# Kernel optimization log

Measured on AMD Instinct MI355X. Metric: run time of the kernel, lower is better.

The kernel has to match this reference:

```python
import jax, jax.numpy as jnp
import numpy as np

D = 128      # d_model
H = 8        # n_heads
HD = D // H  # head_dim = 16
E = 256      # n_experts
R = 32       # kv_lora_rank
B, T = 4, 512
EPS = 1e-6


def _dense_init(k, fi, fo):
    s = float(1.0 / np.sqrt(fi))
    return jax.random.uniform(k, (fi, fo), minval=-s, maxval=s, dtype=jnp.float32)


def setup_inputs() -> dict:
    key = jax.random.key(0)
    ks = jax.random.split(key, 16)
    rng = np.random.RandomState(42)
    Q, _ = np.linalg.qr(rng.randn(D, D))
    glim = float(np.sqrt(6.0 / (D + D)))
    return {
        'x': jax.random.normal(ks[0], (B, T, D), dtype=jnp.float32),
        'g1': jnp.ones((D,), jnp.float32),
        'qW': _dense_init(ks[1], D, D), 'qb': jnp.zeros((D,), jnp.float32),
        'kdW': _dense_init(ks[2], D, R), 'kdb': jnp.zeros((R,), jnp.float32),
        'kuW': _dense_init(ks[3], R, 2 * D), 'kub': jnp.zeros((2 * D,), jnp.float32),
        'oW': _dense_init(ks[4], D, D), 'ob': jnp.zeros((D,), jnp.float32),
        'rot': jnp.asarray(Q, jnp.float32),
        'tq_scale': jnp.ones((D,), jnp.float32),
        's1W': _dense_init(ks[5], D, D), 's1b': jnp.zeros((D,), jnp.float32),
        's2W': _dense_init(ks[6], D, D), 's2b': jnp.zeros((D,), jnp.float32),
        'g2': jnp.ones((D,), jnp.float32),
        'gateW': _dense_init(ks[7], D, E), 'gateb': jnp.zeros((E,), jnp.float32),
        'expW': jax.random.uniform(ks[8], (E, D, D), minval=-glim, maxval=glim, dtype=jnp.float32),
        'm1W': _dense_init(ks[9], D, D), 'm1b': jnp.zeros((D,), jnp.float32),
        'm2W': _dense_init(ks[10], D, D), 'm2b': jnp.zeros((D,), jnp.float32),
    }


def _rmsnorm(x, g):
    return g * (x / jnp.sqrt(jnp.mean(x * x, axis=-1, keepdims=True) + EPS))


def _swiglu(x, w1, b1, w2, b2):
    gate = x @ w1 + b1
    return gate * jax.nn.sigmoid(gate) * (x @ w2 + b2)


def _mla(x, qW, qb, kdW, kdb, kuW, kub, oW, ob):
    b, t = x.shape[0], x.shape[1]
    q = (x @ qW + qb).reshape(b, t, H, HD)
    kv = ((x @ kdW + kdb) @ kuW + kub).reshape(b, t, H, 2 * HD)
    k, v = jnp.split(kv, 2, axis=-1)
    q = jax.nn.elu(q) + 1.0
    k = jax.nn.elu(k) + 1.0
    # linear attention: context[b,h,d,e] = sum_t k[b,t,h,d] v[b,t,h,e]
    context = jnp.einsum('bthd,bthe->bhde', k, v)
    out = jnp.einsum('bthd,bhde->bthe', q, context)
    k_sum = jnp.sum(k, axis=1)  # [b,h,d]
    z = 1.0 / (jnp.einsum('bthd,bhd->bth', q, k_sum) + EPS)
    out = out * z[..., None]
    return out.reshape(b, t, D) @ oW + ob


def _turbo_quant(x, rot, scale):
    x = x @ rot
    mag = jnp.sqrt(jnp.mean(x * x, axis=-1, keepdims=True) + EPS)
    phase = x / mag
    qp = jnp.clip(phase * 127.0, -127.0, 127.0) / 127.0
    phase = jax.lax.stop_gradient(qp - phase) + phase  # straight-through
    return phase * mag * scale


def _moe(h, gateW, gateb, expW, m1W, m1b, m2W, m2b):
    gate_scores = jax.nn.softmax(h @ gateW + gateb, axis=-1)  # [B,T,E]
    top_vals, top_idx = jax.lax.top_k(gate_scores, 2)
    top_w = top_vals / (jnp.sum(top_vals, axis=-1, keepdims=True) + EPS)
    # dense all-expert compute as in the original module
    eo = jnp.einsum('btd,edo->bteo', h, expW)  # [B,T,E,D]
    mask = jnp.sum(jax.nn.one_hot(top_idx, E, dtype=h.dtype) * top_w[..., None], axis=2)  # [B,T,E]
    wavg = jnp.einsum('bteo,bte->bto', eo, mask)
    wavg = _swiglu(wavg, m1W, m1b, m2W, m2b)
    diff_sq = jnp.square(eo - wavg[:, :, None, :])
    wvar = jnp.einsum('bteo,bte->bto', diff_sq, mask)
    consensus = jnp.exp(-jnp.mean(wvar, axis=-1))  # [B,T]
    return wavg, consensus


def reference(x, g1, qW, qb, kdW, kdb, kuW, kub, oW, ob, rot, tq_scale,
              s1W, s1b, s2W, s2b, g2, gateW, gateb, expW, m1W, m1b, m2W, m2b):
    attn_out = _turbo_quant(_mla(_rmsnorm(x, g1), qW, qb, kdW, kdb, kuW, kub, oW, ob), rot, tq_scale)
    x = x + _swiglu(attn_out, s1W, s1b, s2W, s2b)
    moe_out, consensus = _moe(_rmsnorm(x, g2), gateW, gateb, expW, m1W, m1b, m2W, m2b)
    return x + moe_out, consensus
```

## Files before the change

### kernel.cpp

```cpp
#include <hip/hip_runtime.h>
#include <hip/hip_bf16.h>
#include <math.h>

static constexpr int Dd   = 128;
static constexpr int NH   = 8;
static constexpr int HD   = 16;
static constexpr int NE   = 256;
static constexpr int RR   = 32;
static constexpr int BB   = 4;
static constexpr int TT   = 512;
static constexpr int NTOK = BB * TT;
static constexpr int TPB  = 4;
#define EPSF 1e-6f

__device__ __forceinline__ float elu1(float v) { return v > 0.f ? v + 1.f : expf(v); }
__device__ __forceinline__ float sigm(float v) { return 1.f / (1.f + expf(-v)); }

__global__ __launch_bounds__(256) void k_pre(
    const float* __restrict__ x, const float* __restrict__ g1,
    const float* __restrict__ qW, const float* __restrict__ qb,
    const float* __restrict__ kdW, const float* __restrict__ kdb,
    const float* __restrict__ kuW, const float* __restrict__ kub,
    float* __restrict__ qbuf, float* __restrict__ kvbuf,
    float* __restrict__ ctx, float* __restrict__ ksum, int* __restrict__ cnt) {
  const int tid = threadIdx.x;
  const int j = tid & 127, g = tid >> 7;
  const int lane = tid & 63, wid = tid >> 6;
  const int n0 = blockIdx.x * TPB;

  __shared__ float4 h1T[128];
  __shared__ float4 part0[128];
  __shared__ float4 kpart[4][32];
  __shared__ float4 kdT[32];
  __shared__ float4 rtmp[2];

  if (blockIdx.x == 0) {
    for (int i = tid; i < 32 * 256; i += 256) ctx[i] = 0.f;
    for (int i = tid; i < 32 * 16; i += 256) ksum[i] = 0.f;
    cnt[tid] = 0;
  }

  float xv[4];
  if (g == 0) {
    float v[4];
#pragma unroll
    for (int t = 0; t < 4; t++) { xv[t] = x[(n0 + t) * Dd + j]; v[t] = xv[t] * xv[t]; }
#pragma unroll
    for (int o = 32; o > 0; o >>= 1) {
#pragma unroll
      for (int t = 0; t < 4; t++) v[t] += __shfl_xor(v[t], o, 64);
    }
    if (lane == 0) rtmp[wid] = make_float4(v[0], v[1], v[2], v[3]);
  }
  __syncthreads();
  if (g == 0) {
    float g1j = g1[j];
#pragma unroll
    for (int t = 0; t < 4; t++) {
      float ss = ((const float*)&rtmp[0])[t] + ((const float*)&rtmp[1])[t];
      ((float*)&h1T[j])[t] = g1j * xv[t] * rsqrtf(ss * (1.f / 128.f) + EPSF);
    }
  }
  __syncthreads();

  {
    float a0 = 0, a1 = 0, a2 = 0, a3 = 0;
    const float* Wp = qW + (g * 64) * Dd + j;
#pragma unroll 8
    for (int i = 0; i < 64; i++) {
      float4 h4 = h1T[g * 64 + i];
      float w = Wp[i * Dd];
      a0 += h4.x * w; a1 += h4.y * w; a2 += h4.z * w; a3 += h4.w * w;
    }
    if (g == 1) part0[j] = make_float4(a0, a1, a2, a3);
    __syncthreads();
    if (g == 0) {
      float4 p = part0[j];
      float bb = qb[j];
      float q0 = a0 + p.x + bb, q1 = a1 + p.y + bb, q2 = a2 + p.z + bb, q3 = a3 + p.w + bb;
      qbuf[(n0 + 0) * Dd + j] = elu1(q0);
      qbuf[(n0 + 1) * Dd + j] = elu1(q1);
      qbuf[(n0 + 2) * Dd + j] = elu1(q2);
      qbuf[(n0 + 3) * Dd + j] = elu1(q3);
    }
  }

  if (tid < 128) {
    int col = tid & 31, ksp = tid >> 5;
    float a0 = 0, a1 = 0, a2 = 0, a3 = 0;
    const float* Wp = kdW + (ksp * 32) * RR + col;
#pragma unroll 8
    for (int i = 0; i < 32; i++) {
      float4 h4 = h1T[ksp * 32 + i];
      float w = Wp[i * RR];
      a0 += h4.x * w; a1 += h4.y * w; a2 += h4.z * w; a3 += h4.w * w;
    }
    kpart[ksp][col] = make_float4(a0, a1, a2, a3);
  }
  __syncthreads();
  if (tid < 32) {
    float bb = kdb[tid];
    float4 p0 = kpart[0][tid], p1 = kpart[1][tid], p2 = kpart[2][tid], p3 = kpart[3][tid];
    kdT[tid] = make_float4(p0.x + p1.x + p2.x + p3.x + bb,
                           p0.y + p1.y + p2.y + p3.y + bb,
                           p0.z + p1.z + p2.z + p3.z + bb,
                           p0.w + p1.w + p2.w + p3.w + bb);
  }
  __syncthreads();

  {
    float a0 = 0, a1 = 0, a2 = 0, a3 = 0;
    const float* Wp = kuW + tid;
#pragma unroll 8
    for (int r = 0; r < 32; r++) {
      float4 k4 = kdT[r];
      float w = Wp[r * 256];
      a0 += k4.x * w; a1 += k4.y * w; a2 += k4.z * w; a3 += k4.w * w;
    }
    float bb = kub[tid];
    bool isk = (tid & 31) < 16;
    float v0 = a0 + bb, v1 = a1 + bb, v2 = a2 + bb, v3 = a3 + bb;
    kvbuf[(n0 + 0) * 256 + tid] = isk ? elu1(v0) : v0;
    kvbuf[(n0 + 1) * 256 + tid] = isk ? elu1(v1) : v1;
    kvbuf[(n0 + 2) * 256 + tid] = isk ? elu1(v2) : v2;
    kvbuf[(n0 + 3) * 256 + tid] = isk ? elu1(v3) : v3;
  }
}

__global__ __launch_bounds__(256) void k_ctx(const float* __restrict__ kv,
                                             float* __restrict__ ctx,
                                             float* __restrict__ ksum) {
  const int blk = blockIdx.x;
  const int bh = blk >> 3, c = blk & 7;
  const int b = bh >> 3, h = bh & 7;
  const int tid = threadIdx.x;
  const int d = tid >> 4, e = tid & 15;
  __shared__ float sh[64 * 32];
#pragma unroll
  for (int r = 0; r < 8; r++) {
    int lin = r * 256 + tid;
    int tok = lin >> 5, off = lin & 31;
    sh[lin] = kv[((b * TT + c * 64 + tok) * 256) + h * 32 + off];
  }
  __syncthreads();
  float acc = 0.f, ks = 0.f;
#pragma unroll 4
  for (int t = 0; t < 64; t++) {
    float kk = sh[t * 32 + d];
    acc += kk * sh[t * 32 + 16 + e];
    ks += kk;
  }
  atomicAdd(&ctx[bh * 256 + d * 16 + e], acc);
  if (e == 0) atomicAdd(&ksum[bh * 16 + d], ks);
}

__global__ __launch_bounds__(256) void k_mid(
    const float* __restrict__ x, const float* __restrict__ qbuf,
    const float* __restrict__ ctx, const float* __restrict__ ksum,
    const float* __restrict__ oW, const float* __restrict__ ob,
    const float* __restrict__ rot, const float* __restrict__ tqs,
    const float* __restrict__ s1W, const float* __restrict__ s1b,
    const float* __restrict__ s2W, const float* __restrict__ s2b,
    const float* __restrict__ g2, const float* __restrict__ gateW,
    const float* __restrict__ gateb,
    float* __restrict__ xnbuf, float* __restrict__ h2buf,
    float* __restrict__ gw, int* __restrict__ gidx, int* __restrict__ cnt) {
  const int tid = threadIdx.x;
  const int j = tid & 127, g = tid >> 7;
  const int lane = tid & 63, wid2 = (tid >> 6) & 1;
  const int wid4 = tid >> 6;
  const int n0 = blockIdx.x * TPB;
  const int b = n0 >> 9;

  __shared__ float4 bufA[128], bufB[128];
  __shared__ float4 part[2][128];
  __shared__ float4 rtmp[2];
  __shared__ float wvS[4][4]; __shared__ int wiS[4][4];
  __shared__ float zS[4][4];

  {
    float a = qbuf[(n0 + 2 * g) * Dd + j];
    float c = qbuf[(n0 + 2 * g + 1) * Dd + j];
    ((float*)&bufA[j])[2 * g] = a;
    ((float*)&bufA[j])[2 * g + 1] = c;
  }
  __syncthreads();

  if (g == 0) {
    int h = j >> 4, e = j & 15;
    const float* cpt = ctx + (b * NH + h) * 256;
    const float* kpt = ksum + (b * NH + h) * 16;
    float num[4] = {0, 0, 0, 0}, den[4] = {0, 0, 0, 0};
#pragma unroll
    for (int d = 0; d < 16; d++) {
      float cx = cpt[d * 16 + e], ks = kpt[d];
      float4 q4 = bufA[h * 16 + d];
      num[0] += q4.x * cx; num[1] += q4.y * cx; num[2] += q4.z * cx; num[3] += q4.w * cx;
      den[0] += q4.x * ks; den[1] += q4.y * ks; den[2] += q4.z * ks; den[3] += q4.w * ks;
    }
#pragma unroll
    for (int t = 0; t < 4; t++) ((float*)&bufB[j])[t] = num[t] / (den[t] + EPSF);
  }
  __syncthreads();

  {
    float a0 = 0, a1 = 0, a2 = 0, a3 = 0;
    const float* Wp = oW + (g * 64) * Dd + j;
#pragma unroll 8
    for (int i = 0; i < 64; i++) {
      float4 h4 = bufB[g * 64 + i];
      float w = Wp[i * Dd];
      a0 += h4.x * w; a1 += h4.y * w; a2 += h4.z * w; a3 += h4.w * w;
    }
    if (g == 1) part[0][j] = make_float4(a0, a1, a2, a3);
    __syncthreads();
    if (g == 0) {
      float4 p = part[0][j];
      float bb = ob[j];
      bufA[j] = make_float4(a0 + p.x + bb, a1 + p.y + bb, a2 + p.z + bb, a3 + p.w + bb);
    }
    __syncthreads();
  }

  {
    float a0 = 0, a1 = 0, a2 = 0, a3 = 0;
    const float* Wp = rot + (g * 64) * Dd + j;
#pragma unroll 8
    for (int i = 0; i < 64; i++) {
      float4 h4 = bufA[g * 64 + i];
      float w = Wp[i * Dd];
      a0 += h4.x * w; a1 += h4.y * w; a2 += h4.z * w; a3 += h4.w * w;
    }
    if (g == 1) part[0][j] = make_float4(a0, a1, a2, a3);
    __syncthreads();
    float tot[4];
    if (g == 0) {
      float4 p = part[0][j];
      tot[0] = a0 + p.x; tot[1] = a1 + p.y; tot[2] = a2 + p.z; tot[3] = a3 + p.w;
      float v[4];
#pragma unroll
      for (int t = 0; t < 4; t++) v[t] = tot[t] * tot[t];
#pragma unroll
      for (int o = 32; o > 0; o >>= 1) {
#pragma unroll
        for (int t = 0; t < 4; t++) v[t] += __shfl_xor(v[t], o, 64);
      }
      if (lane == 0) rtmp[wid2] = make_float4(v[0], v[1], v[2], v[3]);
    }
    __syncthreads();
    if (g == 0) {
      float scj = tqs[j];
#pragma unroll
      for (int t = 0; t < 4; t++) {
        float ss = ((const float*)&rtmp[0])[t] + ((const float*)&rtmp[1])[t];
        float mag = sqrtf(ss * (1.f / 128.f) + EPSF);
        float ph = tot[t] / mag;
        float p127 = fminf(fmaxf(ph * 127.f, -127.f), 127.f);
        ((float*)&bufB[j])[t] = (p127 * (1.f / 127.f)) * mag * scj;
      }
    }
    __syncthreads();
  }

  {
    float a1v[4] = {0, 0, 0, 0}, a2v[4] = {0, 0, 0, 0};
    const float* W1p = s1W + (g * 64) * Dd + j;
    const float* W2p = s2W + (g * 64) * Dd + j;
#pragma unroll 4
    for (int i = 0; i < 64; i++) {
      float4 h4 = bufB[g * 64 + i];
      float w1 = W1p[i * Dd], w2 = W2p[i * Dd];
      a1v[0] += h4.x * w1; a1v[1] += h4.y * w1; a1v[2] += h4.z * w1; a1v[3] += h4.w * w1;
      a2v[0] += h4.x * w2; a2v[1] += h4.y * w2; a2v[2] += h4.z * w2; a2v[3] += h4.w * w2;
    }
    if (g == 1) {
      part[0][j] = make_float4(a1v[0], a1v[1], a1v[2], a1v[3]);
      part[1][j] = make_float4(a2v[0], a2v[1], a2v[2], a2v[3]);
    }
    __syncthreads();
    float xn[4];
    if (g == 0) {
      float b1 = s1b[j], b2 = s2b[j];
      float4 p1 = part[0][j], p2 = part[1][j];
      float gv[4], uv[4];
      gv[0] = a1v[0] + p1.x + b1; gv[1] = a1v[1] + p1.y + b1;
      gv[2] = a1v[2] + p1.z + b1; gv[3] = a1v[3] + p1.w + b1;
      uv[0] = a2v[0] + p2.x + b2; uv[1] = a2v[1] + p2.y + b2;
      uv[2] = a2v[2] + p2.z + b2; uv[3] = a2v[3] + p2.w + b2;
      float v[4];
#pragma unroll
      for (int t = 0; t < 4; t++) {
        xn[t] = x[(n0 + t) * Dd + j] + gv[t] * sigm(gv[t]) * uv[t];
        xnbuf[(n0 + t) * Dd + j] = xn[t];
        v[t] = xn[t] * xn[t];
      }
#pragma unroll
      for (int o = 32; o > 0; o >>= 1) {
#pragma unroll
        for (int t = 0; t < 4; t++) v[t] += __shfl_xor(v[t], o, 64);
      }
      if (lane == 0) rtmp[wid2] = make_float4(v[0], v[1], v[2], v[3]);
    }
    __syncthreads();
    if (g == 0) {
      float g2j = g2[j];
#pragma unroll
      for (int t = 0; t < 4; t++) {
        float ss = ((const float*)&rtmp[0])[t] + ((const float*)&rtmp[1])[t];
        float h2v = g2j * xn[t] * rsqrtf(ss * (1.f / 128.f) + EPSF);
        ((float*)&bufA[j])[t] = h2v;
        h2buf[(n0 + t) * Dd + j] = h2v;
      }
    }
    __syncthreads();
  }

  float val[4];
  {
    float a0 = 0, a1 = 0, a2 = 0, a3 = 0;
    const float* Wp = gateW + tid;
#pragma unroll 8
    for (int i = 0; i < 128; i++) {
      float4 h4 = bufA[i];
      float w = Wp[i * NE];
      a0 += h4.x * w; a1 += h4.y * w; a2 += h4.z * w; a3 += h4.w * w;
    }
    float bb = gateb[tid];
    val[0] = a0 + bb; val[1] = a1 + bb; val[2] = a2 + bb; val[3] = a3 + bb;
  }

  float m1[4]; int i1[4];
  {
    float bv[4]; int bi[4];
#pragma unroll
    for (int t = 0; t < 4; t++) { bv[t] = val[t]; bi[t] = tid; }
#pragma unroll
    for (int o = 32; o > 0; o >>= 1) {
#pragma unroll
      for (int t = 0; t < 4; t++) {
        float wv = __shfl_xor(bv[t], o, 64);
        int wi = __shfl_xor(bi[t], o, 64);
        if (wv > bv[t] || (wv == bv[t] && wi < bi[t])) { bv[t] = wv; bi[t] = wi; }
      }
    }
    if (lane == 0) {
#pragma unroll
      for (int t = 0; t < 4; t++) { wvS[wid4][t] = bv[t]; wiS[wid4][t] = bi[t]; }
    }
    __syncthreads();
#pragma unroll
    for (int t = 0; t < 4; t++) {
      m1[t] = wvS[0][t]; i1[t] = wiS[0][t];
#pragma unroll
      for (int w = 1; w < 4; w++) {
        float cv = wvS[w][t]; int ci = wiS[w][t];
        if (cv > m1[t] || (cv == m1[t] && ci < i1[t])) { m1[t] = cv; i1[t] = ci; }
      }
    }
    __syncthreads();
  }
  float m2[4]; int i2[4];
  {
    float bv[4]; int bi[4];
#pragma unroll
    for (int t = 0; t < 4; t++) {
      bv[t] = (tid == i1[t]) ? -INFINITY : val[t];
      bi[t] = tid;
    }
#pragma unroll
    for (int o = 32; o > 0; o >>= 1) {
#pragma unroll
      for (int t = 0; t < 4; t++) {
        float wv = __shfl_xor(bv[t], o, 64);
        int wi = __shfl_xor(bi[t], o, 64);
        if (wv > bv[t] || (wv == bv[t] && wi < bi[t])) { bv[t] = wv; bi[t] = wi; }
      }
    }
    if (lane == 0) {
#pragma unroll
      for (int t = 0; t < 4; t++) { wvS[wid4][t] = bv[t]; wiS[wid4][t] = bi[t]; }
    }
    __syncthreads();
#pragma unroll
    for (int t = 0; t < 4; t++) {
      m2[t] = wvS[0][t]; i2[t] = wiS[0][t];
#pragma unroll
      for (int w = 1; w < 4; w++) {
        float cv = wvS[w][t]; int ci = wiS[w][t];
        if (cv > m2[t] || (cv == m2[t] && ci < i2[t])) { m2[t] = cv; i2[t] = ci; }
      }
    }
    __syncthreads();
  }
  {
    float v[4];
#pragma unroll
    for (int t = 0; t < 4; t++) v[t] = expf(val[t] - m1[t]);
#pragma unroll
    for (int o = 32; o > 0; o >>= 1) {
#pragma unroll
      for (int t = 0; t < 4; t++) v[t] += __shfl_xor(v[t], o, 64);
    }
    if (lane == 0) {
#pragma unroll
      for (int t = 0; t < 4; t++) zS[wid4][t] = v[t];
    }
    __syncthreads();
  }
  if (tid < 4) {
    int t = tid;
    float Z = zS[0][t] + zS[1][t] + zS[2][t] + zS[3][t];
    float p1 = 1.f / Z;
    float p2 = expf(m2[t] - m1[t]) / Z;
    float s = p1 + p2 + EPSF;
    gidx[(n0 + t) * 2 + 0] = i1[t];
    gidx[(n0 + t) * 2 + 1] = i2[t];
    gw[(n0 + t) * 2 + 0] = p1 / s;
    gw[(n0 + t) * 2 + 1] = p2 / s;
    atomicAdd(&cnt[i1[t]], 1);
    atomicAdd(&cnt[i2[t]], 1);
  }
}

__global__ __launch_bounds__(256) void k_route(const int* __restrict__ cnt,
                                               const int* __restrict__ gidx,
                                               int* __restrict__ offb,
                                               int* __restrict__ slottok,
                                               int* __restrict__ tokslot) {
  const int tid = threadIdx.x;
  __shared__ int sc[256];
  __shared__ int lcur[256];
  int c = cnt[tid];
  sc[tid] = c;
  __syncthreads();
  for (int o = 1; o < 256; o <<= 1) {
    int a = (tid >= o) ? sc[tid - o] : 0;
    __syncthreads();
    sc[tid] += a;
    __syncthreads();
  }
  int excl = sc[tid] - c;
  offb[tid] = excl;
  lcur[tid] = excl;
  __syncthreads();
  for (int base = 0; base < NTOK; base += 256) {
    int tok = base + tid;
    int e1 = gidx[tok * 2], e2 = gidx[tok * 2 + 1];
    int s1 = atomicAdd(&lcur[e1], 1);
    tokslot[tok * 2] = s1; slottok[s1] = tok;
    int s2 = atomicAdd(&lcur[e2], 1);
    tokslot[tok * 2 + 1] = s2; slottok[s2] = tok;
  }
}

__global__ __launch_bounds__(256) void k_exp(const float* __restrict__ h2buf,
                                             const int* __restrict__ slottok,
                                             const int* __restrict__ cnt,
                                             const int* __restrict__ offb,
                                             const float* __restrict__ expW,
                                             float* __restrict__ ybuf) {
  const int e = blockIdx.x;
  const int n = cnt[e];
  if (n == 0) return;
  const int base = offb[e];
  const int tid = threadIdx.x;
  const int j = tid & 127, g = tid >> 7;
  __shared__ __align__(16) float hT[128][16];
  const float* Wp = expW + (size_t)e * Dd * Dd + j;
  for (int t0 = 0; t0 < n; t0 += 16) {
    int m = n - t0; if (m > 16) m = 16;
    __syncthreads();
    for (int tt = g; tt < m; tt += 2) {
      int tok = slottok[base + t0 + tt];
      hT[j][tt] = h2buf[tok * Dd + j];
    }
    __syncthreads();
    float acc[8] = {0, 0, 0, 0, 0, 0, 0, 0};
#pragma unroll 4
    for (int i = 0; i < 128; i++) {
      float w = Wp[i * Dd];
      const float* hp = &hT[i][g * 8];
      float4 A = *(const float4*)(hp);
      float4 B = *(const float4*)(hp + 4);
      acc[0] += A.x * w; acc[1] += A.y * w; acc[2] += A.z * w; acc[3] += A.w * w;
      acc[4] += B.x * w; acc[5] += B.y * w; acc[6] += B.z * w; acc[7] += B.w * w;
    }
#pragma unroll
    for (int k = 0; k < 8; k++) {
      int tt = g * 8 + k;
      if (tt < m) ybuf[(size_t)(base + t0 + tt) * Dd + j] = acc[k];
    }
  }
}

__global__ __launch_bounds__(256) void k_post(
    const float* __restrict__ xnbuf, const float* __restrict__ ybuf,
    const int* __restrict__ tokslot, const float* __restrict__ gw,
    const float* __restrict__ m1W, const float* __restrict__ m1b,
    const float* __restrict__ m2W, const float* __restrict__ m2b,
    float* __restrict__ out) {
  const int tid = threadIdx.x;
  const int j = tid & 127, g = tid >> 7;
  const int lane = tid & 63, wid2 = (tid >> 6) & 1;
  const int n0 = blockIdx.x * TPB;

  __shared__ float4 y1T[128], y2T[128], inT[128], sT[128];
  __shared__ float4 part[2][128];
  __shared__ float4 rtmp[2];
  __shared__ int sSlot[4][2];
  __shared__ float sWt[4][2];

  if (tid < 4) {
    sSlot[tid][0] = tokslot[(n0 + tid) * 2];
    sSlot[tid][1] = tokslot[(n0 + tid) * 2 + 1];
    sWt[tid][0] = gw[(n0 + tid) * 2];
    sWt[tid][1] = gw[(n0 + tid) * 2 + 1];
  }
  __syncthreads();

#pragma unroll
  for (int tt = 0; tt < 2; tt++) {
    int t = 2 * g + tt;
    float y1 = ybuf[(size_t)sSlot[t][0] * Dd + j];
    float y2 = ybuf[(size_t)sSlot[t][1] * Dd + j];
    ((float*)&y1T[j])[t] = y1;
    ((float*)&y2T[j])[t] = y2;
    ((float*)&inT[j])[t] = sWt[t][0] * y1 + sWt[t][1] * y2;
  }
  __syncthreads();

  {
    float a1v[4] = {0, 0, 0, 0}, a2v[4] = {0, 0, 0, 0};
    const float* W1p = m1W + (g * 64) * Dd + j;
    const float* W2p = m2W + (g * 64) * Dd + j;
#pragma unroll 4
    for (int i = 0; i < 64; i++) {
      float4 h4 = inT[g * 64 + i];
      float w1 = W1p[i * Dd], w2 = W2p[i * Dd];
      a1v[0] += h4.x * w1; a1v[1] += h4.y * w1; a1v[2] += h4.z * w1; a1v[3] += h4.w * w1;
      a2v[0] += h4.x * w2; a2v[1] += h4.y * w2; a2v[2] += h4.z * w2; a2v[3] += h4.w * w2;
    }
    if (g == 1) {
      part[0][j] = make_float4(a1v[0], a1v[1], a1v[2], a1v[3]);
      part[1][j] = make_float4(a2v[0], a2v[1], a2v[2], a2v[3]);
    }
    __syncthreads();
    if (g == 0) {
      float b1 = m1b[j], b2 = m2b[j];
      float4 p1 = part[0][j], p2 = part[1][j];
      float gv[4], uv[4];
      gv[0] = a1v[0] + p1.x + b1; gv[1] = a1v[1] + p1.y + b1;
      gv[2] = a1v[2] + p1.z + b1; gv[3] = a1v[3] + p1.w + b1;
      uv[0] = a2v[0] + p2.x + b2; uv[1] = a2v[1] + p2.y + b2;
      uv[2] = a2v[2] + p2.z + b2; uv[3] = a2v[3] + p2.w + b2;
#pragma unroll
      for (int t = 0; t < 4; t++) {
        float sv = gv[t] * sigm(gv[t]) * uv[t];
        ((float*)&sT[j])[t] = sv;
        out[(n0 + t) * Dd + j] = xnbuf[(n0 + t) * Dd + j] + sv;
      }
    }
    __syncthreads();
  }

  if (g == 0) {
    float v[4];
#pragma unroll
    for (int t = 0; t < 4; t++) {
      float sv = ((const float*)&sT[j])[t];
      float d1 = ((const float*)&y1T[j])[t] - sv;
      float d2 = ((const float*)&y2T[j])[t] - sv;
      v[t] = sWt[t][0] * d1 * d1 + sWt[t][1] * d2 * d2;
    }
#pragma unroll
    for (int o = 32; o > 0; o >>= 1) {
#pragma unroll
      for (int t = 0; t < 4; t++) v[t] += __shfl_xor(v[t], o, 64);
    }
    if (lane == 0) rtmp[wid2] = make_float4(v[0], v[1], v[2], v[3]);
  }
  __syncthreads();
  if (tid < 4) {
    float s = ((const float*)&rtmp[0])[tid] + ((const float*)&rtmp[1])[tid];
    out[NTOK * Dd + n0 + tid] = expf(-s * (1.f / 128.f));
  }
}

extern "C" void kernel_launch(void* const* d_in, const int* in_sizes, int n_in,
                              void* d_out, int out_size, void* d_ws, size_t ws_size,
                              hipStream_t stream) {
  const float* x   = (const float*)d_in[0];
  const float* g1  = (const float*)d_in[1];
  const float* qW  = (const float*)d_in[2];
  const float* qb  = (const float*)d_in[3];
  const float* kdW = (const float*)d_in[4];
  const float* kdb = (const float*)d_in[5];
  const float* kuW = (const float*)d_in[6];
  const float* kub = (const float*)d_in[7];
  const float* oW  = (const float*)d_in[8];
  const float* ob  = (const float*)d_in[9];
  const float* rot = (const float*)d_in[10];
  const float* tqs = (const float*)d_in[11];
  const float* s1W = (const float*)d_in[12];
  const float* s1b = (const float*)d_in[13];
  const float* s2W = (const float*)d_in[14];
  const float* s2b = (const float*)d_in[15];
  const float* g2  = (const float*)d_in[16];
  const float* gW  = (const float*)d_in[17];
  const float* gb  = (const float*)d_in[18];
  const float* eW  = (const float*)d_in[19];
  const float* m1W = (const float*)d_in[20];
  const float* m1b = (const float*)d_in[21];
  const float* m2W = (const float*)d_in[22];
  const float* m2b = (const float*)d_in[23];
  float* out = (float*)d_out;
  float* ws  = (float*)d_ws;

  float* qbuf  = ws;
  float* kvbuf = ws + 262144;
  float* ybuf  = ws;
  float* ctx   = ws + 786432;
  float* ksum  = ctx + 8192;
  float* h2buf = ksum + 512;
  float* xnbuf = h2buf + 262144;
  float* gw    = xnbuf + 262144;
  int*   gidx    = (int*)(gw + 4096);
  int*   cnt     = gidx + 4096;
  int*   offb    = cnt + 256;
  int*   slottok = offb + 256;
  int*   tokslot = slottok + 4096;

  k_pre<<<NTOK / TPB, 256, 0, stream>>>(x, g1, qW, qb, kdW, kdb, kuW, kub,
                                        qbuf, kvbuf, ctx, ksum, cnt);
  k_ctx<<<256, 256, 0, stream>>>(kvbuf, ctx, ksum);
  k_mid<<<NTOK / TPB, 256, 0, stream>>>(x, qbuf, ctx, ksum, oW, ob, rot, tqs,
                                        s1W, s1b, s2W, s2b, g2, gW, gb,
                                        xnbuf, h2buf, gw, gidx, cnt);
  k_route<<<1, 256, 0, stream>>>(cnt, gidx, offb, slottok, tokslot);
  k_exp<<<NE, 256, 0, stream>>>(h2buf, slottok, cnt, offb, eW, ybuf);
  k_post<<<NTOK / TPB, 256, 0, stream>>>(xnbuf, ybuf, tokslot, gw,
                                         m1W, m1b, m2W, m2b, out);
}
```

Before: 195.5 us.

## Double block size to 512 threads with wider K-split reductions

Four kernels (pre, mid, exp, post) move from 256 to 512 threads per block. Each matvec's K dimension is split across four thread groups instead of two, with partial sums reduced through shared memory. The expert GEMM gives each thread 4 tokens instead of 8 and pads its shared tile stride to 20. The aim is more parallel work per block to hide the latency of the serial matvec chains, at the cost of extra shared-memory reductions, more barriers and idle threads in the top-k and softmax stages.

```diff
diff --git a/kernel.cpp b/kernel.cpp
--- a/kernel.cpp
+++ b/kernel.cpp
@@ -16,7 +16,7 @@
 __device__ __forceinline__ float elu1(float v) { return v > 0.f ? v + 1.f : expf(v); }
 __device__ __forceinline__ float sigm(float v) { return 1.f / (1.f + expf(-v)); }
 
-__global__ __launch_bounds__(256) void k_pre(
+__global__ __launch_bounds__(512) void k_pre(
     const float* __restrict__ x, const float* __restrict__ g1,
     const float* __restrict__ qW, const float* __restrict__ qb,
     const float* __restrict__ kdW, const float* __restrict__ kdb,
@@ -25,23 +25,24 @@
     float* __restrict__ ctx, float* __restrict__ ksum, int* __restrict__ cnt) {
   const int tid = threadIdx.x;
   const int j = tid & 127, g = tid >> 7;
-  const int lane = tid & 63, wid = tid >> 6;
+  const int lane = tid & 63;
   const int n0 = blockIdx.x * TPB;
 
   __shared__ float4 h1T[128];
-  __shared__ float4 part0[128];
-  __shared__ float4 kpart[4][32];
+  __shared__ float4 part[3][128];
+  __shared__ float4 kpart[8][32];
   __shared__ float4 kdT[32];
+  __shared__ float4 kupart[256];
   __shared__ float4 rtmp[2];
 
   if (blockIdx.x == 0) {
-    for (int i = tid; i < 32 * 256; i += 256) ctx[i] = 0.f;
-    for (int i = tid; i < 32 * 16; i += 256) ksum[i] = 0.f;
-    cnt[tid] = 0;
+    for (int i = tid; i < 32 * 256; i += 512) ctx[i] = 0.f;
+    ksum[tid] = 0.f;
+    if (tid < 256) cnt[tid] = 0;
   }
 
   float xv[4];
-  if (g == 0) {
+  if (tid < 128) {
     float v[4];
 #pragma unroll
     for (int t = 0; t < 4; t++) { xv[t] = x[(n0 + t) * Dd + j]; v[t] = xv[t] * xv[t]; }
@@ -50,10 +51,10 @@
 #pragma unroll
       for (int t = 0; t < 4; t++) v[t] += __shfl_xor(v[t], o, 64);
     }
-    if (lane == 0) rtmp[wid] = make_float4(v[0], v[1], v[2], v[3]);
-  }
-  __syncthreads();
-  if (g == 0) {
+    if (lane == 0) rtmp[tid >> 6] = make_float4(v[0], v[1], v[2], v[3]);
+  }
+  __syncthreads();
+  if (tid < 128) {
     float g1j = g1[j];
 #pragma unroll
     for (int t = 0; t < 4; t++) {
@@ -65,33 +66,33 @@
 
   {
     float a0 = 0, a1 = 0, a2 = 0, a3 = 0;
-    const float* Wp = qW + (g * 64) * Dd + j;
-#pragma unroll 8
-    for (int i = 0; i < 64; i++) {
-      float4 h4 = h1T[g * 64 + i];
+    const float* Wp = qW + (g * 32) * Dd + j;
+#pragma unroll 16
+    for (int i = 0; i < 32; i++) {
+      float4 h4 = h1T[g * 32 + i];
       float w = Wp[i * Dd];
       a0 += h4.x * w; a1 += h4.y * w; a2 += h4.z * w; a3 += h4.w * w;
     }
-    if (g == 1) part0[j] = make_float4(a0, a1, a2, a3);
+    if (g) part[g - 1][j] = make_float4(a0, a1, a2, a3);
     __syncthreads();
     if (g == 0) {
-      float4 p = part0[j];
+      float4 p0 = part[0][j], p1 = part[1][j], p2 = part[2][j];
       float bb = qb[j];
-      float q0 = a0 + p.x + bb, q1 = a1 + p.y + bb, q2 = a2 + p.z + bb, q3 = a3 + p.w + bb;
-      qbuf[(n0 + 0) * Dd + j] = elu1(q0);
-      qbuf[(n0 + 1) * Dd + j] = elu1(q1);
-      qbuf[(n0 + 2) * Dd + j] = elu1(q2);
-      qbuf[(n0 + 3) * Dd + j] = elu1(q3);
-    }
-  }
-
-  if (tid < 128) {
+      qbuf[(n0 + 0) * Dd + j] = elu1(a0 + p0.x + p1.x + p2.x + bb);
+      qbuf[(n0 + 1) * Dd + j] = elu1(a1 + p0.y + p1.y + p2.y + bb);
+      qbuf[(n0 + 2) * Dd + j] = elu1(a2 + p0.z + p1.z + p2.z + bb);
+      qbuf[(n0 + 3) * Dd + j] = elu1(a3 + p0.w + p1.w + p2.w + bb);
+    }
+    __syncthreads();
+  }
+
+  if (tid < 256) {
     int col = tid & 31, ksp = tid >> 5;
     float a0 = 0, a1 = 0, a2 = 0, a3 = 0;
-    const float* Wp = kdW + (ksp * 32) * RR + col;
-#pragma unroll 8
-    for (int i = 0; i < 32; i++) {
-      float4 h4 = h1T[ksp * 32 + i];
+    const float* Wp = kdW + (ksp * 16) * RR + col;
+#pragma unroll
+    for (int i = 0; i < 16; i++) {
+      float4 h4 = h1T[ksp * 16 + i];
       float w = Wp[i * RR];
       a0 += h4.x * w; a1 += h4.y * w; a2 += h4.z * w; a3 += h4.w * w;
     }
@@ -100,30 +101,38 @@
   __syncthreads();
   if (tid < 32) {
     float bb = kdb[tid];
-    float4 p0 = kpart[0][tid], p1 = kpart[1][tid], p2 = kpart[2][tid], p3 = kpart[3][tid];
-    kdT[tid] = make_float4(p0.x + p1.x + p2.x + p3.x + bb,
-                           p0.y + p1.y + p2.y + p3.y + bb,
-                           p0.z + p1.z + p2.z + p3.z + bb,
-                           p0.w + p1.w + p2.w + p3.w + bb);
-  }
-  __syncthreads();
-
-  {
-    float a0 = 0, a1 = 0, a2 = 0, a3 = 0;
-    const float* Wp = kuW + tid;
-#pragma unroll 8
-    for (int r = 0; r < 32; r++) {
-      float4 k4 = kdT[r];
+    float s0 = bb, s1 = bb, s2 = bb, s3 = bb;
+#pragma unroll
+    for (int k = 0; k < 8; k++) {
+      float4 p = kpart[k][tid];
+      s0 += p.x; s1 += p.y; s2 += p.z; s3 += p.w;
+    }
+    kdT[tid] = make_float4(s0, s1, s2, s3);
+  }
+  __syncthreads();
+
+  {
+    int col = tid & 255, kh = tid >> 8;
+    float a0 = 0, a1 = 0, a2 = 0, a3 = 0;
+    const float* Wp = kuW + (kh * 16) * 256 + col;
+#pragma unroll
+    for (int r = 0; r < 16; r++) {
+      float4 k4 = kdT[kh * 16 + r];
       float w = Wp[r * 256];
       a0 += k4.x * w; a1 += k4.y * w; a2 += k4.z * w; a3 += k4.w * w;
     }
-    float bb = kub[tid];
-    bool isk = (tid & 31) < 16;
-    float v0 = a0 + bb, v1 = a1 + bb, v2 = a2 + bb, v3 = a3 + bb;
-    kvbuf[(n0 + 0) * 256 + tid] = isk ? elu1(v0) : v0;
-    kvbuf[(n0 + 1) * 256 + tid] = isk ? elu1(v1) : v1;
-    kvbuf[(n0 + 2) * 256 + tid] = isk ? elu1(v2) : v2;
-    kvbuf[(n0 + 3) * 256 + tid] = isk ? elu1(v3) : v3;
+    if (kh) kupart[col] = make_float4(a0, a1, a2, a3);
+    __syncthreads();
+    if (!kh) {
+      float4 p = kupart[col];
+      float bb = kub[col];
+      bool isk = (col & 31) < 16;
+      float v0 = a0 + p.x + bb, v1 = a1 + p.y + bb, v2 = a2 + p.z + bb, v3 = a3 + p.w + bb;
+      kvbuf[(n0 + 0) * 256 + col] = isk ? elu1(v0) : v0;
+      kvbuf[(n0 + 1) * 256 + col] = isk ? elu1(v1) : v1;
+      kvbuf[(n0 + 2) * 256 + col] = isk ? elu1(v2) : v2;
+      kvbuf[(n0 + 3) * 256 + col] = isk ? elu1(v3) : v3;
+    }
   }
 }
 
@@ -154,7 +163,7 @@
   if (e == 0) atomicAdd(&ksum[bh * 16 + d], ks);
 }
 
-__global__ __launch_bounds__(256) void k_mid(
+__global__ __launch_bounds__(512) void k_mid(
     const float* __restrict__ x, const float* __restrict__ qbuf,
     const float* __restrict__ ctx, const float* __restrict__ ksum,
     const float* __restrict__ oW, const float* __restrict__ ob,
@@ -167,26 +176,21 @@
     float* __restrict__ gw, int* __restrict__ gidx, int* __restrict__ cnt) {
   const int tid = threadIdx.x;
   const int j = tid & 127, g = tid >> 7;
-  const int lane = tid & 63, wid2 = (tid >> 6) & 1;
-  const int wid4 = tid >> 6;
+  const int lane = tid & 63;
   const int n0 = blockIdx.x * TPB;
   const int b = n0 >> 9;
 
   __shared__ float4 bufA[128], bufB[128];
-  __shared__ float4 part[2][128];
+  __shared__ float4 part[3][128];
+  __shared__ float4 gpart[256];
   __shared__ float4 rtmp[2];
   __shared__ float wvS[4][4]; __shared__ int wiS[4][4];
   __shared__ float zS[4][4];
 
-  {
-    float a = qbuf[(n0 + 2 * g) * Dd + j];
-    float c = qbuf[(n0 + 2 * g + 1) * Dd + j];
-    ((float*)&bufA[j])[2 * g] = a;
-    ((float*)&bufA[j])[2 * g + 1] = c;
-  }
-  __syncthreads();
-
-  if (g == 0) {
+  ((float*)&bufA[j])[g] = qbuf[(n0 + g) * Dd + j];
+  __syncthreads();
+
+  if (tid < 128) {
     int h = j >> 4, e = j & 15;
     const float* cpt = ctx + (b * NH + h) * 256;
     const float* kpt = ksum + (b * NH + h) * 16;
@@ -205,38 +209,40 @@
 
   {
     float a0 = 0, a1 = 0, a2 = 0, a3 = 0;
-    const float* Wp = oW + (g * 64) * Dd + j;
-#pragma unroll 8
-    for (int i = 0; i < 64; i++) {
-      float4 h4 = bufB[g * 64 + i];
+    const float* Wp = oW + (g * 32) * Dd + j;
+#pragma unroll 16
+    for (int i = 0; i < 32; i++) {
+      float4 h4 = bufB[g * 32 + i];
       float w = Wp[i * Dd];
       a0 += h4.x * w; a1 += h4.y * w; a2 += h4.z * w; a3 += h4.w * w;
     }
-    if (g == 1) part[0][j] = make_float4(a0, a1, a2, a3);
+    if (g) part[g - 1][j] = make_float4(a0, a1, a2, a3);
     __syncthreads();
     if (g == 0) {
-      float4 p = part[0][j];
+      float4 p0 = part[0][j], p1 = part[1][j], p2 = part[2][j];
       float bb = ob[j];
-      bufA[j] = make_float4(a0 + p.x + bb, a1 + p.y + bb, a2 + p.z + bb, a3 + p.w + bb);
-    }
-    __syncthreads();
-  }
-
-  {
-    float a0 = 0, a1 = 0, a2 = 0, a3 = 0;
-    const float* Wp = rot + (g * 64) * Dd + j;
-#pragma unroll 8
-    for (int i = 0; i < 64; i++) {
-      float4 h4 = bufA[g * 64 + i];
+      bufA[j] = make_float4(a0 + p0.x + p1.x + p2.x + bb, a1 + p0.y + p1.y + p2.y + bb,
+                            a2 + p0.z + p1.z + p2.z + bb, a3 + p0.w + p1.w + p2.w + bb);
+    }
+    __syncthreads();
+  }
+
+  {
+    float a0 = 0, a1 = 0, a2 = 0, a3 = 0;
+    const float* Wp = rot + (g * 32) * Dd + j;
+#pragma unroll 16
+    for (int i = 0; i < 32; i++) {
+      float4 h4 = bufA[g * 32 + i];
       float w = Wp[i * Dd];
       a0 += h4.x * w; a1 += h4.y * w; a2 += h4.z * w; a3 += h4.w * w;
     }
-    if (g == 1) part[0][j] = make_float4(a0, a1, a2, a3);
+    if (g) part[g - 1][j] = make_float4(a0, a1, a2, a3);
     __syncthreads();
     float tot[4];
     if (g == 0) {
-      float4 p = part[0][j];
-      tot[0] = a0 + p.x; tot[1] = a1 + p.y; tot[2] = a2 + p.z; tot[3] = a3 + p.w;
+      float4 p0 = part[0][j], p1 = part[1][j], p2 = part[2][j];
+      tot[0] = a0 + p0.x + p1.x + p2.x; tot[1] = a1 + p0.y + p1.y + p2.y;
+      tot[2] = a2 + p0.z + p1.z + p2.z; tot[3] = a3 + p0.w + p1.w + p2.w;
       float v[4];
 #pragma unroll
       for (int t = 0; t < 4; t++) v[t] = tot[t] * tot[t];
@@ -245,7 +251,7 @@
 #pragma unroll
         for (int t = 0; t < 4; t++) v[t] += __shfl_xor(v[t], o, 64);
       }
-      if (lane == 0) rtmp[wid2] = make_float4(v[0], v[1], v[2], v[3]);
+      if (lane == 0) rtmp[tid >> 6] = make_float4(v[0], v[1], v[2], v[3]);
     }
     __syncthreads();
     if (g == 0) {
@@ -263,30 +269,25 @@
   }
 
   {
-    float a1v[4] = {0, 0, 0, 0}, a2v[4] = {0, 0, 0, 0};
-    const float* W1p = s1W + (g * 64) * Dd + j;
-    const float* W2p = s2W + (g * 64) * Dd + j;
-#pragma unroll 4
+    float a0 = 0, a1 = 0, a2 = 0, a3 = 0;
+    const float* Wp = (g < 2 ? s1W : s2W) + ((g & 1) * 64) * Dd + j;
+#pragma unroll 16
     for (int i = 0; i < 64; i++) {
-      float4 h4 = bufB[g * 64 + i];
-      float w1 = W1p[i * Dd], w2 = W2p[i * Dd];
-      a1v[0] += h4.x * w1; a1v[1] += h4.y * w1; a1v[2] += h4.z * w1; a1v[3] += h4.w * w1;
-      a2v[0] += h4.x * w2; a2v[1] += h4.y * w2; a2v[2] += h4.z * w2; a2v[3] += h4.w * w2;
-    }
-    if (g == 1) {
-      part[0][j] = make_float4(a1v[0], a1v[1], a1v[2], a1v[3]);
-      part[1][j] = make_float4(a2v[0], a2v[1], a2v[2], a2v[3]);
-    }
+      float4 h4 = bufB[(g & 1) * 64 + i];
+      float w = Wp[i * Dd];
+      a0 += h4.x * w; a1 += h4.y * w; a2 += h4.z * w; a3 += h4.w * w;
+    }
+    if (g) part[g - 1][j] = make_float4(a0, a1, a2, a3);
     __syncthreads();
     float xn[4];
     if (g == 0) {
       float b1 = s1b[j], b2 = s2b[j];
-      float4 p1 = part[0][j], p2 = part[1][j];
+      float4 p0 = part[0][j], p1 = part[1][j], p2 = part[2][j];
       float gv[4], uv[4];
-      gv[0] = a1v[0] + p1.x + b1; gv[1] = a1v[1] + p1.y + b1;
-      gv[2] = a1v[2] + p1.z + b1; gv[3] = a1v[3] + p1.w + b1;
-      uv[0] = a2v[0] + p2.x + b2; uv[1] = a2v[1] + p2.y + b2;
-      uv[2] = a2v[2] + p2.z + b2; uv[3] = a2v[3] + p2.w + b2;
+      gv[0] = a0 + p0.x + b1; gv[1] = a1 + p0.y + b1;
+      gv[2] = a2 + p0.z + b1; gv[3] = a3 + p0.w + b1;
+      uv[0] = p1.x + p2.x + b2; uv[1] = p1.y + p2.y + b2;
+      uv[2] = p1.z + p2.z + b2; uv[3] = p1.w + p2.w + b2;
       float v[4];
 #pragma unroll
       for (int t = 0; t < 4; t++) {
@@ -299,7 +300,7 @@
 #pragma unroll
         for (int t = 0; t < 4; t++) v[t] += __shfl_xor(v[t], o, 64);
       }
-      if (lane == 0) rtmp[wid2] = make_float4(v[0], v[1], v[2], v[3]);
+      if (lane == 0) rtmp[tid >> 6] = make_float4(v[0], v[1], v[2], v[3]);
     }
     __syncthreads();
     if (g == 0) {
@@ -317,93 +318,111 @@
 
   float val[4];
   {
-    float a0 = 0, a1 = 0, a2 = 0, a3 = 0;
-    const float* Wp = gateW + tid;
-#pragma unroll 8
-    for (int i = 0; i < 128; i++) {
-      float4 h4 = bufA[i];
+    int col = tid & 255, kh = tid >> 8;
+    float a0 = 0, a1 = 0, a2 = 0, a3 = 0;
+    const float* Wp = gateW + (kh * 64) * NE + col;
+#pragma unroll 16
+    for (int i = 0; i < 64; i++) {
+      float4 h4 = bufA[kh * 64 + i];
       float w = Wp[i * NE];
       a0 += h4.x * w; a1 += h4.y * w; a2 += h4.z * w; a3 += h4.w * w;
     }
-    float bb = gateb[tid];
-    val[0] = a0 + bb; val[1] = a1 + bb; val[2] = a2 + bb; val[3] = a3 + bb;
-  }
+    if (kh) gpart[col] = make_float4(a0, a1, a2, a3);
+    __syncthreads();
+    if (!kh) {
+      float4 p = gpart[col];
+      float bb = gateb[col];
+      val[0] = a0 + p.x + bb; val[1] = a1 + p.y + bb;
+      val[2] = a2 + p.z + bb; val[3] = a3 + p.w + bb;
+    }
+  }
+  __syncthreads();
 
   float m1[4]; int i1[4];
   {
-    float bv[4]; int bi[4];
-#pragma unroll
-    for (int t = 0; t < 4; t++) { bv[t] = val[t]; bi[t] = tid; }
-#pragma unroll
-    for (int o = 32; o > 0; o >>= 1) {
+    if (tid < 256) {
+      float bv[4]; int bi[4];
+#pragma unroll
+      for (int t = 0; t < 4; t++) { bv[t] = val[t]; bi[t] = tid; }
+#pragma unroll
+      for (int o = 32; o > 0; o >>= 1) {
+#pragma unroll
+        for (int t = 0; t < 4; t++) {
+          float wv = __shfl_xor(bv[t], o, 64);
+          int wi = __shfl_xor(bi[t], o, 64);
+          if (wv > bv[t] || (wv == bv[t] && wi < bi[t])) { bv[t] = wv; bi[t] = wi; }
+        }
+      }
+      if (lane == 0) {
+#pragma unroll
+        for (int t = 0; t < 4; t++) { wvS[tid >> 6][t] = bv[t]; wiS[tid >> 6][t] = bi[t]; }
+      }
+    }
+    __syncthreads();
+    if (tid < 256) {
 #pragma unroll
       for (int t = 0; t < 4; t++) {
-        float wv = __shfl_xor(bv[t], o, 64);
-        int wi = __shfl_xor(bi[t], o, 64);
-        if (wv > bv[t] || (wv == bv[t] && wi < bi[t])) { bv[t] = wv; bi[t] = wi; }
-      }
-    }
-    if (lane == 0) {
-#pragma unroll
-      for (int t = 0; t < 4; t++) { wvS[wid4][t] = bv[t]; wiS[wid4][t] = bi[t]; }
-    }
-    __syncthreads();
-#pragma unroll
-    for (int t = 0; t < 4; t++) {
-      m1[t] = wvS[0][t]; i1[t] = wiS[0][t];
-#pragma unroll
-      for (int w = 1; w < 4; w++) {
-        float cv = wvS[w][t]; int ci = wiS[w][t];
-        if (cv > m1[t] || (cv == m1[t] && ci < i1[t])) { m1[t] = cv; i1[t] = ci; }
+        m1[t] = wvS[0][t]; i1[t] = wiS[0][t];
+#pragma unroll
+        for (int w = 1; w < 4; w++) {
+          float cv = wvS[w][t]; int ci = wiS[w][t];
+          if (cv > m1[t] || (cv == m1[t] && ci < i1[t])) { m1[t] = cv; i1[t] = ci; }
+        }
       }
     }
     __syncthreads();
   }
   float m2[4]; int i2[4];
   {
-    float bv[4]; int bi[4];
-#pragma unroll
-    for (int t = 0; t < 4; t++) {
-      bv[t] = (tid == i1[t]) ? -INFINITY : val[t];
-      bi[t] = tid;
-    }
-#pragma unroll
-    for (int o = 32; o > 0; o >>= 1) {
+    if (tid < 256) {
+      float bv[4]; int bi[4];
 #pragma unroll
       for (int t = 0; t < 4; t++) {
-        float wv = __shfl_xor(bv[t], o, 64);
-        int wi = __shfl_xor(bi[t], o, 64);
-        if (wv > bv[t] || (wv == bv[t] && wi < bi[t])) { bv[t] = wv; bi[t] = wi; }
-      }
-    }
-    if (lane == 0) {
-#pragma unroll
-      for (int t = 0; t < 4; t++) { wvS[wid4][t] = bv[t]; wiS[wid4][t] = bi[t]; }
-    }
-    __syncthreads();
-#pragma unroll
-    for (int t = 0; t < 4; t++) {
-      m2[t] = wvS[0][t]; i2[t] = wiS[0][t];
-#pragma unroll
-      for (int w = 1; w < 4; w++) {
-        float cv = wvS[w][t]; int ci = wiS[w][t];
-        if (cv > m2[t] || (cv == m2[t] && ci < i2[t])) { m2[t] = cv; i2[t] = ci; }
-      }
-    }
-    __syncthreads();
-  }
-  {
-    float v[4];
-#pragma unroll
-    for (int t = 0; t < 4; t++) v[t] = expf(val[t] - m1[t]);
-#pragma unroll
-    for (int o = 32; o > 0; o >>= 1) {
-#pragma unroll
-      for (int t = 0; t < 4; t++) v[t] += __shfl_xor(v[t], o, 64);
-    }
-    if (lane == 0) {
-#pragma unroll
-      for (int t = 0; t < 4; t++) zS[wid4][t] = v[t];
+        bv[t] = (tid == i1[t]) ? -INFINITY : val[t];
+        bi[t] = tid;
+      }
+#pragma unroll
+      for (int o = 32; o > 0; o >>= 1) {
+#pragma unroll
+        for (int t = 0; t < 4; t++) {
+          float wv = __shfl_xor(bv[t], o, 64);
+          int wi = __shfl_xor(bi[t], o, 64);
+          if (wv > bv[t] || (wv == bv[t] && wi < bi[t])) { bv[t] = wv; bi[t] = wi; }
+        }
+      }
+      if (lane == 0) {
+#pragma unroll
+        for (int t = 0; t < 4; t++) { wvS[tid >> 6][t] = bv[t]; wiS[tid >> 6][t] = bi[t]; }
+      }
+    }
+    __syncthreads();
+    if (tid < 256) {
+#pragma unroll
+      for (int t = 0; t < 4; t++) {
+        m2[t] = wvS[0][t]; i2[t] = wiS[0][t];
+#pragma unroll
+        for (int w = 1; w < 4; w++) {
+          float cv = wvS[w][t]; int ci = wiS[w][t];
+          if (cv > m2[t] || (cv == m2[t] && ci < i2[t])) { m2[t] = cv; i2[t] = ci; }
+        }
+      }
+    }
+    __syncthreads();
+  }
+  {
+    if (tid < 256) {
+      float v[4];
+#pragma unroll
+      for (int t = 0; t < 4; t++) v[t] = expf(val[t] - m1[t]);
+#pragma unroll
+      for (int o = 32; o > 0; o >>= 1) {
+#pragma unroll
+        for (int t = 0; t < 4; t++) v[t] += __shfl_xor(v[t], o, 64);
+      }
+      if (lane == 0) {
+#pragma unroll
+        for (int t = 0; t < 4; t++) zS[tid >> 6][t] = v[t];
+      }
     }
     __syncthreads();
   }
@@ -453,7 +472,7 @@
   }
 }
 
-__global__ __launch_bounds__(256) void k_exp(const float* __restrict__ h2buf,
+__global__ __launch_bounds__(512) void k_exp(const float* __restrict__ h2buf,
                                              const int* __restrict__ slottok,
                                              const int* __restrict__ cnt,
                                              const int* __restrict__ offb,
@@ -465,35 +484,32 @@
   const int base = offb[e];
   const int tid = threadIdx.x;
   const int j = tid & 127, g = tid >> 7;
-  __shared__ __align__(16) float hT[128][16];
+  __shared__ __align__(16) float hT[128 * 20];
   const float* Wp = expW + (size_t)e * Dd * Dd + j;
   for (int t0 = 0; t0 < n; t0 += 16) {
     int m = n - t0; if (m > 16) m = 16;
     __syncthreads();
-    for (int tt = g; tt < m; tt += 2) {
+    for (int tt = g; tt < m; tt += 4) {
       int tok = slottok[base + t0 + tt];
-      hT[j][tt] = h2buf[tok * Dd + j];
-    }
-    __syncthreads();
-    float acc[8] = {0, 0, 0, 0, 0, 0, 0, 0};
-#pragma unroll 4
+      hT[j * 20 + tt] = h2buf[tok * Dd + j];
+    }
+    __syncthreads();
+    float acc[4] = {0, 0, 0, 0};
+#pragma unroll 8
     for (int i = 0; i < 128; i++) {
       float w = Wp[i * Dd];
-      const float* hp = &hT[i][g * 8];
-      float4 A = *(const float4*)(hp);
-      float4 B = *(const float4*)(hp + 4);
-      acc[0] += A.x * w; acc[1] += A.y * w; acc[2] += A.z * w; acc[3] += A.w * w;
-      acc[4] += B.x * w; acc[5] += B.y * w; acc[6] += B.z * w; acc[7] += B.w * w;
-    }
-#pragma unroll
-    for (int k = 0; k < 8; k++) {
-      int tt = g * 8 + k;
+      float4 h4 = *(const float4*)&hT[i * 20 + g * 4];
+      acc[0] += h4.x * w; acc[1] += h4.y * w; acc[2] += h4.z * w; acc[3] += h4.w * w;
+    }
+#pragma unroll
+    for (int k = 0; k < 4; k++) {
+      int tt = g * 4 + k;
       if (tt < m) ybuf[(size_t)(base + t0 + tt) * Dd + j] = acc[k];
     }
   }
 }
 
-__global__ __launch_bounds__(256) void k_post(
+__global__ __launch_bounds__(512) void k_post(
     const float* __restrict__ xnbuf, const float* __restrict__ ybuf,
     const int* __restrict__ tokslot, const float* __restrict__ gw,
     const float* __restrict__ m1W, const float* __restrict__ m1b,
@@ -501,11 +517,11 @@
     float* __restrict__ out) {
   const int tid = threadIdx.x;
   const int j = tid & 127, g = tid >> 7;
-  const int lane = tid & 63, wid2 = (tid >> 6) & 1;
+  const int lane = tid & 63;
   const int n0 = blockIdx.x * TPB;
 
   __shared__ float4 y1T[128], y2T[128], inT[128], sT[128];
-  __shared__ float4 part[2][128];
+  __shared__ float4 part[3][128];
   __shared__ float4 rtmp[2];
   __shared__ int sSlot[4][2];
   __shared__ float sWt[4][2];
@@ -518,41 +534,34 @@
   }
   __syncthreads();
 
-#pragma unroll
-  for (int tt = 0; tt < 2; tt++) {
-    int t = 2 * g + tt;
-    float y1 = ybuf[(size_t)sSlot[t][0] * Dd + j];
-    float y2 = ybuf[(size_t)sSlot[t][1] * Dd + j];
-    ((float*)&y1T[j])[t] = y1;
-    ((float*)&y2T[j])[t] = y2;
-    ((float*)&inT[j])[t] = sWt[t][0] * y1 + sWt[t][1] * y2;
-  }
-  __syncthreads();
-
-  {
-    float a1v[4] = {0, 0, 0, 0}, a2v[4] = {0, 0, 0, 0};
-    const float* W1p = m1W + (g * 64) * Dd + j;
-    const float* W2p = m2W + (g * 64) * Dd + j;
-#pragma unroll 4
+  {
+    float y1 = ybuf[(size_t)sSlot[g][0] * Dd + j];
+    float y2 = ybuf[(size_t)sSlot[g][1] * Dd + j];
+    ((float*)&y1T[j])[g] = y1;
+    ((float*)&y2T[j])[g] = y2;
+    ((float*)&inT[j])[g] = sWt[g][0] * y1 + sWt[g][1] * y2;
+  }
+  __syncthreads();
+
+  {
+    float a0 = 0, a1 = 0, a2 = 0, a3 = 0;
+    const float* Wp = (g < 2 ? m1W : m2W) + ((g & 1) * 64) * Dd + j;
+#pragma unroll 16
     for (int i = 0; i < 64; i++) {
-      float4 h4 = inT[g * 64 + i];
-      float w1 = W1p[i * Dd], w2 = W2p[i * Dd];
-      a1v[0] += h4.x * w1; a1v[1] += h4.y * w1; a1v[2] += h4.z * w1; a1v[3] += h4.w * w1;
-      a2v[0] += h4.x * w2; a2v[1] += h4.y * w2; a2v[2] += h4.z * w2; a2v[3] += h4.w * w2;
-    }
-    if (g == 1) {
-      part[0][j] = make_float4(a1v[0], a1v[1], a1v[2], a1v[3]);
-      part[1][j] = make_float4(a2v[0], a2v[1], a2v[2], a2v[3]);
-    }
+      float4 h4 = inT[(g & 1) * 64 + i];
+      float w = Wp[i * Dd];
+      a0 += h4.x * w; a1 += h4.y * w; a2 += h4.z * w; a3 += h4.w * w;
+    }
+    if (g) part[g - 1][j] = make_float4(a0, a1, a2, a3);
     __syncthreads();
     if (g == 0) {
       float b1 = m1b[j], b2 = m2b[j];
-      float4 p1 = part[0][j], p2 = part[1][j];
+      float4 p0 = part[0][j], p1 = part[1][j], p2 = part[2][j];
       float gv[4], uv[4];
-      gv[0] = a1v[0] + p1.x + b1; gv[1] = a1v[1] + p1.y + b1;
-      gv[2] = a1v[2] + p1.z + b1; gv[3] = a1v[3] + p1.w + b1;
-      uv[0] = a2v[0] + p2.x + b2; uv[1] = a2v[1] + p2.y + b2;
-      uv[2] = a2v[2] + p2.z + b2; uv[3] = a2v[3] + p2.w + b2;
+      gv[0] = a0 + p0.x + b1; gv[1] = a1 + p0.y + b1;
+      gv[2] = a2 + p0.z + b1; gv[3] = a3 + p0.w + b1;
+      uv[0] = p1.x + p2.x + b2; uv[1] = p1.y + p2.y + b2;
+      uv[2] = p1.z + p2.z + b2; uv[3] = p1.w + p2.w + b2;
 #pragma unroll
       for (int t = 0; t < 4; t++) {
         float sv = gv[t] * sigm(gv[t]) * uv[t];
@@ -563,7 +572,7 @@
     __syncthreads();
   }
 
-  if (g == 0) {
+  if (tid < 128) {
     float v[4];
 #pragma unroll
     for (int t = 0; t < 4; t++) {
@@ -577,7 +586,7 @@
 #pragma unroll
       for (int t = 0; t < 4; t++) v[t] += __shfl_xor(v[t], o, 64);
     }
-    if (lane == 0) rtmp[wid2] = make_float4(v[0], v[1], v[2], v[3]);
+    if (lane == 0) rtmp[tid >> 6] = make_float4(v[0], v[1], v[2], v[3]);
   }
   __syncthreads();
   if (tid < 4) {
@@ -630,14 +639,14 @@
   int*   slottok = offb + 256;
   int*   tokslot = slottok + 4096;
 
-  k_pre<<<NTOK / TPB, 256, 0, stream>>>(x, g1, qW, qb, kdW, kdb, kuW, kub,
+  k_pre<<<NTOK / TPB, 512, 0, stream>>>(x, g1, qW, qb, kdW, kdb, kuW, kub,
                                         qbuf, kvbuf, ctx, ksum, cnt);
   k_ctx<<<256, 256, 0, stream>>>(kvbuf, ctx, ksum);
-  k_mid<<<NTOK / TPB, 256, 0, stream>>>(x, qbuf, ctx, ksum, oW, ob, rot, tqs,
+  k_mid<<<NTOK / TPB, 512, 0, stream>>>(x, qbuf, ctx, ksum, oW, ob, rot, tqs,
                                         s1W, s1b, s2W, s2b, g2, gW, gb,
                                         xnbuf, h2buf, gw, gidx, cnt);
   k_route<<<1, 256, 0, stream>>>(cnt, gidx, offb, slottok, tokslot);
-  k_exp<<<NE, 256, 0, stream>>>(h2buf, slottok, cnt, offb, eW, ybuf);
-  k_post<<<NTOK / TPB, 256, 0, stream>>>(xnbuf, ybuf, tokslot, gw,
+  k_exp<<<NE, 512, 0, stream>>>(h2buf, slottok, cnt, offb, eW, ybuf);
+  k_post<<<NTOK / TPB, 512, 0, stream>>>(xnbuf, ybuf, tokslot, gw,
                                          m1W, m1b, m2W, m2b, out);
 }
```

New measurement: 172.1 us. -12.0%, faster.
